# Optimization experiments

Measured on AMD Instinct MI355X. Metric: run time of the kernel, lower is better.

Reference implementation:

```python
import jax, jax.numpy as jnp
import numpy as np

B, SEQ, DIM = 4, 8192, 512
G = 32              # group_size: number of outer chunks (per source rearrange 'b (g n) d')
QK = 128            # query_key_dim
HD = QK // 4        # head_dim = 32 (used for softmax scale)
HEAD_D = 2 * HD     # per-head feature dim = 64 (h=2 heads over QK)
HID = DIM           # expansion_factor = 1.0
EPS = 1e-5


def _shift_seq(t):
    # F.pad(t, (0,0,1,-1)): prepend one zero row along axis=-2, drop last row
    pad = [(0, 0)] * (t.ndim - 2) + [(1, 0), (0, 0)]
    return jnp.pad(t, pad)[..., :-1, :]


def setup_inputs() -> dict:
    key = jax.random.key(0)
    ks = jax.random.split(key, 8)
    s = 0.02
    return {
        "x": jax.random.normal(ks[0], (B, SEQ, DIM), jnp.float32),
        "ln_g": jnp.ones((DIM,), jnp.float32),
        "ln_b": jnp.zeros((DIM,), jnp.float32),
        "w_qk": jax.random.normal(ks[1], (DIM, QK), jnp.float32) * s,
        "g4": jax.random.normal(ks[2], (4, QK), jnp.float32) * s,   # qk_offset_scale.gamma
        "b4": jnp.zeros((4, QK), jnp.float32),                       # qk_offset_scale.beta
        "g2": jax.random.normal(ks[3], (2, QK), jnp.float32) * s,   # shift_one_offset_scale.gamma
        "b2": jnp.zeros((2, QK), jnp.float32),
        "w_hidden": jax.random.normal(ks[4], (DIM, 2 * HID), jnp.float32) * s,
        "w_gate": jax.random.normal(ks[5], (DIM, HID), jnp.float32) * s,
        "w_out": jax.random.normal(ks[6], (5 * HID, DIM), jnp.float32) * s,
    }


def reference(x, ln_g, ln_b, w_qk, g4, b4, g2, b2, w_hidden, w_gate, w_out):
    b, seq, dim = x.shape
    n = seq // G  # tokens per chunk; seq chosen as multiple of G so padding = 0

    # LayerNorm
    mu = jnp.mean(x, axis=-1, keepdims=True)
    var = jnp.var(x, axis=-1, keepdims=True)
    xs = (x - mu) * jax.lax.rsqrt(var + EPS) * ln_g + ln_b

    # token shift of first half of channels (shift_tokens=True)
    half = dim // 2
    xs = jnp.concatenate([_shift_seq(xs[..., :half]), xs[..., half:]], axis=-1)

    qk = xs @ w_qk                                  # [b, seq, QK]
    qk_g = qk.reshape(b, G, n, QK)                  # 'b (g n) d -> b g n d', g outer
    qk_mean = qk_g.mean(axis=2)                     # [b, G, QK]

    # OffsetScale(heads=4) on per-chunk mean -> q_offset, k_offset, q_scale, k_scale
    offs = qk_mean[:, :, None, :] * g4 + b4         # [b, G, 4, QK]
    q_off, k_off, q_sc, k_sc = (offs[:, :, i, :] for i in range(4))

    q = qk_g * q_sc[:, :, None, :] + q_off[:, :, None, :]   # [b, G, n, QK]
    k = qk_g * k_sc[:, :, None, :] + k_off[:, :, None, :]

    # shift-by-one variants within each chunk, re-scaled + shift-one offsets
    q_s_off = qk_mean * g2[0] + b2[0]               # [b, G, QK]
    k_s_off = qk_mean * g2[1] + b2[1]
    qs = _shift_seq(q) * q_sc[:, :, None, :] + q_s_off[:, :, None, :]
    ks_ = _shift_seq(k) * k_sc[:, :, None, :] + k_s_off[:, :, None, :]

    def heads(t):  # [b,G,n,QK] -> [b,G,2,n,HEAD_D]
        return t.reshape(b, G, n, 2, HEAD_D).transpose(0, 1, 3, 2, 4)

    q_all = jnp.concatenate([heads(q), heads(qs)], axis=2)   # [b,G,4,n,64]
    k_all = jnp.concatenate([heads(k), heads(ks_)], axis=2)

    hg = xs @ w_hidden                              # [b, seq, 2*HID]
    hidden, gate = hg[..., :HID], hg[..., HID:]
    hidden_g = hidden.reshape(b, G, n, HID)

    sim = jnp.einsum('bghid,bghjd->bghij', q_all, k_all) * (HD ** -0.5)
    neg = -jnp.finfo(sim.dtype).max
    causal = jnp.triu(jnp.ones((n, n), dtype=bool), 1)  # applied unconditionally in source
    sim = jnp.where(causal, neg, sim)
    attn = jax.nn.softmax(sim, axis=-1)             # dropout=0 (eval)

    out = jnp.einsum('bghij,bgje->bghie', attn, hidden_g)   # [b,G,4,n,HID]
    gate_g = gate.reshape(b, G, n, HID)
    out = jax.nn.silu(out) * gate_g[:, :, None, :, :]
    out = out.transpose(0, 1, 3, 2, 4).reshape(b, seq, 4 * HID)  # 'b g h n e -> b (g n) (h e)'

    residual = jnp.concatenate([hidden, out], axis=-1)       # [b, seq, 5*HID]
    out = residual @ w_out                                   # [b, seq, dim]
    out = out * jax.nn.silu(xs @ w_gate)
    return out + xs
```

## Files before the change

kernel.cpp:

```cpp
#include <hip/hip_runtime.h>
#include <hip/hip_bf16.h>
#include <math.h>

#define BB 4
#define SEQ 8192
#define DIM 512
#define GG 32
#define NPG 256
#define QKD 128
#define HIDD 512

typedef unsigned short u16;
typedef unsigned int u32;

using s16x8 = __attribute__((ext_vector_type(8))) short;
using f32x4 = __attribute__((ext_vector_type(4))) float;

__device__ __forceinline__ float bf2f(u16 u) { return __uint_as_float(((u32)u) << 16); }
__device__ __forceinline__ u16 f2bf(float f) {
  u32 b = __float_as_uint(f);
  return (u16)((b + 0x7FFFu + ((b >> 16) & 1u)) >> 16);
}
__device__ __forceinline__ float silu_f(float x) { return x / (1.f + expf(-x)); }
__device__ __forceinline__ float silu_fast(float x) { return x / (1.f + __expf(-x)); }
__device__ __forceinline__ float4 fma4(float4 a, float4 b, float4 c) {
  return make_float4(a.x*b.x+c.x, a.y*b.y+c.y, a.z*b.z+c.z, a.w*b.w+c.w);
}
__device__ __forceinline__ float4 mul4(float4 a, float4 b) {
  return make_float4(a.x*b.x, a.y*b.y, a.z*b.z, a.w*b.w);
}
#define LD4(p, off) (*(const float4*)((p) + (off)))

__device__ __forceinline__ s16x8 aff8(s16x8 v, float4 s0, float4 s1, float4 o0, float4 o1) {
  union U { s16x8 x; u16 u[8]; };
  U in; in.x = v; U r;
  r.u[0] = f2bf(bf2f(in.u[0]) * s0.x + o0.x);
  r.u[1] = f2bf(bf2f(in.u[1]) * s0.y + o0.y);
  r.u[2] = f2bf(bf2f(in.u[2]) * s0.z + o0.z);
  r.u[3] = f2bf(bf2f(in.u[3]) * s0.w + o0.w);
  r.u[4] = f2bf(bf2f(in.u[4]) * s1.x + o1.x);
  r.u[5] = f2bf(bf2f(in.u[5]) * s1.y + o1.y);
  r.u[6] = f2bf(bf2f(in.u[6]) * s1.z + o1.z);
  r.u[7] = f2bf(bf2f(in.u[7]) * s1.w + o1.w);
  return r.x;
}
__device__ __forceinline__ s16x8 pack8(float4 a, float4 b) {
  union { s16x8 v; u16 u[8]; } z;
  z.u[0] = f2bf(a.x); z.u[1] = f2bf(a.y); z.u[2] = f2bf(a.z); z.u[3] = f2bf(a.w);
  z.u[4] = f2bf(b.x); z.u[5] = f2bf(b.y); z.u[6] = f2bf(b.z); z.u[7] = f2bf(b.w);
  return z.v;
}

__global__ __launch_bounds__(256) void k_ln(const float* __restrict__ x,
    const float* __restrict__ lg, const float* __restrict__ lb, float* __restrict__ xs) {
  const int row = blockIdx.x;
  const int s = row & (SEQ - 1);
  const int t = threadIdx.x;
  const float* xr = x + (size_t)row * DIM;
  float v0 = xr[t], v1 = xr[t + 256];
  float sum = v0 + v1, sq = v0 * v0 + v1 * v1;
  #pragma unroll
  for (int o = 32; o; o >>= 1) { sum += __shfl_down(sum, o); sq += __shfl_down(sq, o); }
  __shared__ float sm[8];
  const int w = t >> 6;
  if ((t & 63) == 0) { sm[w] = sum; sm[4 + w] = sq; }
  __syncthreads();
  if (t == 0) {
    float S = sm[0] + sm[1] + sm[2] + sm[3];
    float Q = sm[4] + sm[5] + sm[6] + sm[7];
    float mu = S * (1.f / DIM);
    float var = Q * (1.f / DIM) - mu * mu;
    sm[0] = mu; sm[4] = rsqrtf(var + 1e-5f);
  }
  __syncthreads();
  const float mu = sm[0], rs = sm[4];
  float y0 = (v0 - mu) * rs * lg[t] + lb[t];
  float y1 = (v1 - mu) * rs * lg[t + 256] + lb[t + 256];
  xs[(size_t)row * DIM + t + 256] = y1;
  if (s + 1 < SEQ) xs[(size_t)(row + 1) * DIM + t] = y0;
  if (s == 0) xs[(size_t)row * DIM + t] = 0.f;
}

__global__ __launch_bounds__(256) void k_trw(const float* __restrict__ src, u16* __restrict__ dst,
    int N, int dstLD, int rowOff) {
  __shared__ u16 T[64][66];
  const int t = threadIdx.x;
  const int k0 = blockIdx.x * 64, n0 = blockIdx.y * 64;
  #pragma unroll
  for (int i = 0; i < 16; ++i) {
    int idx = t + 256 * i;
    int r = idx >> 6, c = idx & 63;
    T[c][r] = f2bf(src[(size_t)(k0 + r) * N + n0 + c]);
  }
  __syncthreads();
  #pragma unroll
  for (int i = 0; i < 16; ++i) {
    int idx = t + 256 * i;
    int r = idx >> 6, c = idx & 63;
    dst[(size_t)(rowOff + n0 + r) * dstLD + k0 + c] = T[r][c];
  }
}

__global__ __launch_bounds__(256) void k_trh(const u16* __restrict__ hidt, u16* __restrict__ hidr) {
  __shared__ u16 T[64][66];
  const int t = threadIdx.x;
  const int j0 = blockIdx.x * 64;
  const int e0 = blockIdx.y * 64;
  const int bg = blockIdx.z;
  #pragma unroll
  for (int i = 0; i < 16; ++i) {
    int idx = t + 256 * i; int r = idx >> 6, c = idx & 63;
    T[c][r] = hidt[((size_t)bg * 512 + e0 + r) * 256 + j0 + c];
  }
  __syncthreads();
  #pragma unroll
  for (int i = 0; i < 16; ++i) {
    int idx = t + 256 * i; int r = idx >> 6, c = idx & 63;
    hidr[((size_t)bg * 256 + j0 + r) * 512 + e0 + c] = T[r][c];
  }
}

__global__ __launch_bounds__(256, 2) void k_gemm1m(const float* __restrict__ xs,
    const u16* __restrict__ w1t, u16* __restrict__ qk, u16* __restrict__ hidt,
    u16* __restrict__ gate, u16* __restrict__ xg) {
  __shared__ u16 As[128][72];
  __shared__ u16 Bs[128][72];
  const int t = threadIdx.x;
  const int m0 = blockIdx.x * 128, n0 = blockIdx.y * 128;
  const int w = t >> 6, l = t & 63, lr = l & 15, lq = l >> 4;
  const int wr = (w >> 1) * 64, wc = (w & 1) * 64;
  const int sr = t >> 3;
  const int sk = (t & 7) * 8;
  f32x4 acc[4][4];
  #pragma unroll
  for (int i = 0; i < 4; ++i)
    #pragma unroll
    for (int j = 0; j < 4; ++j) acc[i][j] = (f32x4){0.f, 0.f, 0.f, 0.f};
  for (int k0 = 0; k0 < 512; k0 += 64) {
    s16x8 aS[4], bS[4];
    #pragma unroll
    for (int it = 0; it < 4; ++it) {
      const float* ap = xs + (size_t)(m0 + sr + it * 32) * 512 + k0 + sk;
      float4 f0 = *(const float4*)ap;
      float4 f1 = *(const float4*)(ap + 4);
      s16x8 v;
      v[0] = (short)f2bf(f0.x); v[1] = (short)f2bf(f0.y); v[2] = (short)f2bf(f0.z); v[3] = (short)f2bf(f0.w);
      v[4] = (short)f2bf(f1.x); v[5] = (short)f2bf(f1.y); v[6] = (short)f2bf(f1.z); v[7] = (short)f2bf(f1.w);
      aS[it] = v;
      bS[it] = *(const s16x8*)(w1t + (size_t)(n0 + sr + it * 32) * 512 + k0 + sk);
    }
    __syncthreads();
    #pragma unroll
    for (int it = 0; it < 4; ++it) {
      *(s16x8*)&As[sr + it * 32][sk] = aS[it];
      *(s16x8*)&Bs[sr + it * 32][sk] = bS[it];
    }
    __syncthreads();
    #pragma unroll
    for (int kk = 0; kk < 64; kk += 32) {
      s16x8 af[4], bf[4];
      #pragma unroll
      for (int fi = 0; fi < 4; ++fi) af[fi] = *(const s16x8*)&As[wr + fi * 16 + lr][kk + 8 * lq];
      #pragma unroll
      for (int fj = 0; fj < 4; ++fj) bf[fj] = *(const s16x8*)&Bs[wc + fj * 16 + lr][kk + 8 * lq];
      #pragma unroll
      for (int fi = 0; fi < 4; ++fi)
        #pragma unroll
        for (int fj = 0; fj < 4; ++fj)
          acc[fi][fj] = __builtin_amdgcn_mfma_f32_16x16x32_bf16(af[fi], bf[fj], acc[fi][fj], 0, 0, 0);
    }
  }
  if (n0 == 0) {
    #pragma unroll
    for (int fi = 0; fi < 4; ++fi)
      #pragma unroll
      for (int fj = 0; fj < 4; ++fj) {
        const int n = wc + fj * 16 + lr;
        const int mb = m0 + wr + fi * 16 + lq * 4;
        #pragma unroll
        for (int r = 0; r < 4; ++r)
          qk[(size_t)(mb + r) * QKD + n] = f2bf(acc[fi][fj][r]);
      }
  } else if (n0 < 640) {
    const int bg = m0 >> 8;
    #pragma unroll
    for (int fi = 0; fi < 4; ++fi)
      #pragma unroll
      for (int fj = 0; fj < 4; ++fj) {
        const int e = n0 - 128 + wc + fj * 16 + lr;
        const int j0 = (m0 & 255) + wr + fi * 16 + lq * 4;
        ushort4 pk;
        pk.x = f2bf(acc[fi][fj][0]); pk.y = f2bf(acc[fi][fj][1]);
        pk.z = f2bf(acc[fi][fj][2]); pk.w = f2bf(acc[fi][fj][3]);
        *(ushort4*)(hidt + ((size_t)bg * 512 + e) * 256 + j0) = pk;
      }
  } else if (n0 < 1152) {
    #pragma unroll
    for (int fi = 0; fi < 4; ++fi)
      #pragma unroll
      for (int fj = 0; fj < 4; ++fj) {
        const int n = n0 - 640 + wc + fj * 16 + lr;
        const int mb = m0 + wr + fi * 16 + lq * 4;
        #pragma unroll
        for (int r = 0; r < 4; ++r)
          gate[(size_t)(mb + r) * HIDD + n] = f2bf(acc[fi][fj][r]);
      }
  } else {
    #pragma unroll
    for (int fi = 0; fi < 4; ++fi)
      #pragma unroll
      for (int fj = 0; fj < 4; ++fj) {
        const int n = n0 - 1152 + wc + fj * 16 + lr;
        const int mb = m0 + wr + fi * 16 + lq * 4;
        #pragma unroll
        for (int r = 0; r < 4; ++r)
          xg[(size_t)(mb + r) * HIDD + n] = f2bf(silu_f(acc[fi][fj][r]));
      }
  }
}

__global__ __launch_bounds__(128) void k_qkmean(const u16* __restrict__ qk, float* __restrict__ qm) {
  const int bg = blockIdx.x;
  const int c = threadIdx.x;
  const u16* p = qk + (size_t)bg * NPG * QKD + c;
  float s = 0.f;
  for (int i = 0; i < NPG; ++i) s += bf2f(p[(size_t)i * QKD]);
  qm[(size_t)bg * QKD + c] = s * (1.f / NPG);
}

__global__ __launch_bounds__(256, 4) void k_attn(const u16* __restrict__ qk,
    const float* __restrict__ qm, const float* __restrict__ g4, const float* __restrict__ b4,
    const float* __restrict__ g2, const float* __restrict__ b2,
    const u16* __restrict__ hidt, const u16* __restrict__ gate, u16* __restrict__ out4) {
  __shared__ u16 Vs[64][264];
  const int t = threadIdx.x;
  const int l = t & 63;
  const int h = t >> 6;
  const bool sh = (h >= 2);
  const int blk = blockIdx.x;
  const int xcd = blk & 7;
  const int bb = blk >> 3;
  const int bg = xcd * 16 + (bb >> 4);
  const int iw = 15 - (bb & 15);
  const size_t grpRow = (size_t)bg * NPG;
  const int cbase = (h & 1) << 6;
  const int lr = l & 15, lq = l >> 4;
  const int cA = cbase + 8 * lq;
  const int ntmax = iw, jtmax = iw >> 1;
  const int irow = iw * 16 + lr;
  const float* qmp = qm + bg * QKD;
  float4 qmA = LD4(qmp, cA),      qmB = LD4(qmp, cA + 4);
  float4 qmC = LD4(qmp, cA + 32), qmD = LD4(qmp, cA + 36);
  float4 qscA = fma4(qmA, LD4(g4, 2*QKD+cA),    LD4(b4, 2*QKD+cA));
  float4 qscB = fma4(qmB, LD4(g4, 2*QKD+cA+4),  LD4(b4, 2*QKD+cA+4));
  float4 qscC = fma4(qmC, LD4(g4, 2*QKD+cA+32), LD4(b4, 2*QKD+cA+32));
  float4 qscD = fma4(qmD, LD4(g4, 2*QKD+cA+36), LD4(b4, 2*QKD+cA+36));
  float4 qofA = fma4(qmA, LD4(g4, cA),      LD4(b4, cA));
  float4 qofB = fma4(qmB, LD4(g4, cA+4),    LD4(b4, cA+4));
  float4 qofC = fma4(qmC, LD4(g4, cA+32),   LD4(b4, cA+32));
  float4 qofD = fma4(qmD, LD4(g4, cA+36),   LD4(b4, cA+36));
  float4 kscA = fma4(qmA, LD4(g4, 3*QKD+cA),    LD4(b4, 3*QKD+cA));
  float4 kscB = fma4(qmB, LD4(g4, 3*QKD+cA+4),  LD4(b4, 3*QKD+cA+4));
  float4 kscC = fma4(qmC, LD4(g4, 3*QKD+cA+32), LD4(b4, 3*QKD+cA+32));
  float4 kscD = fma4(qmD, LD4(g4, 3*QKD+cA+36), LD4(b4, 3*QKD+cA+36));
  float4 kofA = fma4(qmA, LD4(g4, QKD+cA),      LD4(b4, QKD+cA));
  float4 kofB = fma4(qmB, LD4(g4, QKD+cA+4),    LD4(b4, QKD+cA+4));
  float4 kofC = fma4(qmC, LD4(g4, QKD+cA+32),   LD4(b4, QKD+cA+32));
  float4 kofD = fma4(qmD, LD4(g4, QKD+cA+36),   LD4(b4, QKD+cA+36));
  s16x8 qz0 = {0,0,0,0,0,0,0,0}, qz1 = qz0, kz0 = qz0, kz1 = qz0;
  if (sh) {
    float4 qsoA = fma4(qmA, LD4(g2, cA),    LD4(b2, cA));
    float4 qsoB = fma4(qmB, LD4(g2, cA+4),  LD4(b2, cA+4));
    float4 qsoC = fma4(qmC, LD4(g2, cA+32), LD4(b2, cA+32));
    float4 qsoD = fma4(qmD, LD4(g2, cA+36), LD4(b2, cA+36));
    float4 ksoA = fma4(qmA, LD4(g2, QKD+cA),    LD4(b2, QKD+cA));
    float4 ksoB = fma4(qmB, LD4(g2, QKD+cA+4),  LD4(b2, QKD+cA+4));
    float4 ksoC = fma4(qmC, LD4(g2, QKD+cA+32), LD4(b2, QKD+cA+32));
    float4 ksoD = fma4(qmD, LD4(g2, QKD+cA+36), LD4(b2, QKD+cA+36));
    qofA = fma4(qofA, qscA, qsoA); qofB = fma4(qofB, qscB, qsoB);
    qofC = fma4(qofC, qscC, qsoC); qofD = fma4(qofD, qscD, qsoD);
    qscA = mul4(qscA, qscA); qscB = mul4(qscB, qscB);
    qscC = mul4(qscC, qscC); qscD = mul4(qscD, qscD);
    kofA = fma4(kofA, kscA, ksoA); kofB = fma4(kofB, kscB, ksoB);
    kofC = fma4(kofC, kscC, ksoC); kofD = fma4(kofD, kscD, ksoD);
    kscA = mul4(kscA, kscA); kscB = mul4(kscB, kscB);
    kscC = mul4(kscC, kscC); kscD = mul4(kscD, kscD);
    qz0 = pack8(qsoA, qsoB); qz1 = pack8(qsoC, qsoD);
    kz0 = pack8(ksoA, ksoB); kz1 = pack8(ksoC, ksoD);
  }
  const float scl = 0.17677669529663687f;
  const int qsrc = sh ? (irow ? irow - 1 : 0) : irow;
  const u16* qrow = qk + (grpRow + qsrc) * QKD + cA;
  s16x8 qb0 = aff8(*(const s16x8*)qrow,        qscA, qscB, qofA, qofB);
  s16x8 qb1 = aff8(*(const s16x8*)(qrow + 32), qscC, qscD, qofC, qofD);
  if (sh && irow == 0) { qb0 = qz0; qb1 = qz1; }
  f32x4 sfr[16];
  #pragma unroll
  for (int nt = 0; nt < 16; ++nt) if (nt <= ntmax) {
    const int jr = nt * 16 + lr;
    const int ksrc = sh ? (jr ? jr - 1 : 0) : jr;
    const u16* kr = qk + (grpRow + ksrc) * QKD + cA;
    s16x8 ka0 = aff8(*(const s16x8*)kr,        kscA, kscB, kofA, kofB);
    s16x8 ka1 = aff8(*(const s16x8*)(kr + 32), kscC, kscD, kofC, kofD);
    if (sh && jr == 0) { ka0 = kz0; ka1 = kz1; }
    f32x4 c = {0.f, 0.f, 0.f, 0.f};
    c = __builtin_amdgcn_mfma_f32_16x16x32_bf16(ka0, qb0, c, 0, 0, 0);
    c = __builtin_amdgcn_mfma_f32_16x16x32_bf16(ka1, qb1, c, 0, 0, 0);
    sfr[nt] = c;
  }
  float mx = -3.4e38f;
  #pragma unroll
  for (int nt = 0; nt < 16; ++nt) if (nt <= ntmax) {
    #pragma unroll
    for (int r = 0; r < 4; ++r) {
      int j = nt * 16 + lq * 4 + r;
      if (j <= irow) mx = fmaxf(mx, sfr[nt][r] * scl);
    }
  }
  mx = fmaxf(mx, __shfl_xor(mx, 16));
  mx = fmaxf(mx, __shfl_xor(mx, 32));
  float sum = 0.f;
  u32 p01[16], p23[16];
  #pragma unroll
  for (int nt = 0; nt < 16; ++nt) { p01[nt] = 0u; p23[nt] = 0u; }
  #pragma unroll
  for (int nt = 0; nt < 16; ++nt) if (nt <= ntmax) {
    int j = nt * 16 + lq * 4;
    float e0 = (j + 0 <= irow) ? __expf(sfr[nt][0] * scl - mx) : 0.f;
    float e1 = (j + 1 <= irow) ? __expf(sfr[nt][1] * scl - mx) : 0.f;
    float e2 = (j + 2 <= irow) ? __expf(sfr[nt][2] * scl - mx) : 0.f;
    float e3 = (j + 3 <= irow) ? __expf(sfr[nt][3] * scl - mx) : 0.f;
    sum += (e0 + e1) + (e2 + e3);
    p01[nt] = (u32)f2bf(e0) | ((u32)f2bf(e1) << 16);
    p23[nt] = (u32)f2bf(e2) | ((u32)f2bf(e3) << 16);
  }
  sum += __shfl_xor(sum, 16);
  sum += __shfl_xor(sum, 32);
  const float inv = 1.f / sum;
  const int srcA = (l & 15) | ((l & 16) << 1);
  const int srcB = srcA + 16;
  const bool hi = (l >= 32);
  s16x8 bfr[8];
  #pragma unroll
  for (int jt = 0; jt < 8; ++jt) if (jt <= jtmax) {
    u32 a0 = __shfl((int)p01[2 * jt], srcA), a1 = __shfl((int)p23[2 * jt], srcA);
    u32 a2 = __shfl((int)p01[2 * jt], srcB), a3 = __shfl((int)p23[2 * jt], srcB);
    u32 b0 = __shfl((int)p01[2 * jt + 1], srcA), b1 = __shfl((int)p23[2 * jt + 1], srcA);
    u32 b2 = __shfl((int)p01[2 * jt + 1], srcB), b3 = __shfl((int)p23[2 * jt + 1], srcB);
    union { u32 u[4]; s16x8 v; } bb2;
    bb2.u[0] = hi ? b0 : a0; bb2.u[1] = hi ? b1 : a1;
    bb2.u[2] = hi ? b2 : a2; bb2.u[3] = hi ? b3 : a3;
    bfr[jt] = bb2.v;
  }
  const u16* vtb = hidt + (size_t)bg * (512 * 256);
  const size_t srow = grpRow + irow;
  const u16* gp = gate + srow * HIDD;
  u16* op = out4 + srow * 2048 + ((size_t)h << 9);
  for (int oct = 0; oct < 8; ++oct) {
    __syncthreads();
    const u16* src = vtb + (size_t)oct * 64 * 256;
    #pragma unroll
    for (int it = 0; it < 8; ++it) {
      int flat = it * 256 + t;
      int row = flat >> 5, col8 = (flat & 31) * 8;
      *(uint4*)&Vs[row][col8] = *(const uint4*)(src + (size_t)row * 256 + col8);
    }
    __syncthreads();
    f32x4 acc[4];
    #pragma unroll
    for (int ef = 0; ef < 4; ++ef) acc[ef] = (f32x4){0.f, 0.f, 0.f, 0.f};
    #pragma unroll
    for (int jt = 0; jt < 8; ++jt) if (jt <= jtmax) {
      __builtin_amdgcn_s_setprio(1);
      #pragma unroll
      for (int ef = 0; ef < 4; ++ef) {
        s16x8 va = *(const s16x8*)&Vs[ef * 16 + lr][jt * 32 + 8 * lq];
        acc[ef] = __builtin_amdgcn_mfma_f32_16x16x32_bf16(va, bfr[jt], acc[ef], 0, 0, 0);
      }
      __builtin_amdgcn_s_setprio(0);
    }
    #pragma unroll
    for (int ef = 0; ef < 4; ++ef) {
      const int e = oct * 64 + ef * 16 + lq * 4;
      ushort4 gu = *(const ushort4*)(gp + e);
      ushort4 ov;
      ov.x = f2bf(silu_fast(acc[ef][0] * inv) * bf2f(gu.x));
      ov.y = f2bf(silu_fast(acc[ef][1] * inv) * bf2f(gu.y));
      ov.z = f2bf(silu_fast(acc[ef][2] * inv) * bf2f(gu.z));
      ov.w = f2bf(silu_fast(acc[ef][3] * inv) * bf2f(gu.w));
      *(ushort4*)(op + e) = ov;
    }
  }
}

__global__ __launch_bounds__(256, 2) void k_gemm2m(const u16* __restrict__ hidr,
    const u16* __restrict__ out4, const u16* __restrict__ wt,
    const u16* __restrict__ xg, float* __restrict__ out) {
  __shared__ u16 As[128][72];
  __shared__ u16 Bs[128][72];
  const int t = threadIdx.x;
  const int m0 = blockIdx.x * 128, n0 = blockIdx.y * 128;
  const int w = t >> 6, l = t & 63, lr = l & 15, lq = l >> 4;
  const int wr = (w >> 1) * 64, wc = (w & 1) * 64;
  const int sr = t >> 3;
  const int sk = (t & 7) * 8;
  f32x4 acc[4][4];
  #pragma unroll
  for (int i = 0; i < 4; ++i)
    #pragma unroll
    for (int j = 0; j < 4; ++j) acc[i][j] = (f32x4){0.f, 0.f, 0.f, 0.f};
  for (int k0 = 0; k0 < 2560; k0 += 64) {
    const u16* abase; size_t ald; int koff;
    if (k0 < 512) { abase = hidr; ald = 512; koff = k0; }
    else          { abase = out4; ald = 2048; koff = k0 - 512; }
    s16x8 aS[4], bS[4];
    #pragma unroll
    for (int it = 0; it < 4; ++it) {
      aS[it] = *(const s16x8*)(abase + (size_t)(m0 + sr + it * 32) * ald + koff + sk);
      bS[it] = *(const s16x8*)(wt + (size_t)(n0 + sr + it * 32) * 2560 + k0 + sk);
    }
    __syncthreads();
    #pragma unroll
    for (int it = 0; it < 4; ++it) {
      *(s16x8*)&As[sr + it * 32][sk] = aS[it];
      *(s16x8*)&Bs[sr + it * 32][sk] = bS[it];
    }
    __syncthreads();
    #pragma unroll
    for (int kk = 0; kk < 64; kk += 32) {
      s16x8 af[4], bf[4];
      #pragma unroll
      for (int fi = 0; fi < 4; ++fi) af[fi] = *(const s16x8*)&As[wr + fi * 16 + lr][kk + 8 * lq];
      #pragma unroll
      for (int fj = 0; fj < 4; ++fj) bf[fj] = *(const s16x8*)&Bs[wc + fj * 16 + lr][kk + 8 * lq];
      #pragma unroll
      for (int fi = 0; fi < 4; ++fi)
        #pragma unroll
        for (int fj = 0; fj < 4; ++fj)
          acc[fi][fj] = __builtin_amdgcn_mfma_f32_16x16x32_bf16(af[fi], bf[fj], acc[fi][fj], 0, 0, 0);
    }
  }
  #pragma unroll
  for (int fi = 0; fi < 4; ++fi)
    #pragma unroll
    for (int fj = 0; fj < 4; ++fj) {
      const int n = n0 + wc + fj * 16 + lr;
      const int mb = m0 + wr + fi * 16 + lq * 4;
      #pragma unroll
      for (int r = 0; r < 4; ++r) {
        const size_t idx = (size_t)(mb + r) * DIM + n;
        out[idx] = acc[fi][fj][r] * bf2f(xg[idx]) + out[idx];
      }
    }
}

extern "C" void kernel_launch(void* const* d_in, const int* in_sizes, int n_in,
                              void* d_out, int out_size, void* d_ws, size_t ws_size,
                              hipStream_t stream) {
  const float* x        = (const float*)d_in[0];
  const float* lg       = (const float*)d_in[1];
  const float* lb       = (const float*)d_in[2];
  const float* w_qk     = (const float*)d_in[3];
  const float* g4       = (const float*)d_in[4];
  const float* b4       = (const float*)d_in[5];
  const float* g2       = (const float*)d_in[6];
  const float* b2       = (const float*)d_in[7];
  const float* w_hidden = (const float*)d_in[8];
  const float* w_gate   = (const float*)d_in[9];
  const float* w_out    = (const float*)d_in[10];
  if (ws_size < 247660544ull) return;
  char* ws = (char*)d_ws;
  float* QM   = (float*)(ws + 0);
  u16*   HIDT = (u16*)  (ws + 65536);
  u16*   GATE = (u16*)  (ws + 33619968);
  u16*   XG   = (u16*)  (ws + 67174400);
  u16*   QKb  = (u16*)  (ws + 100728832);
  u16*   W1T  = (u16*)  (ws + 109117440);
  u16*   WT   = (u16*)  (ws + 110821376);
  u16*   OUT4 = (u16*)  (ws + 113442816);
  u16*   HIDR = (u16*)  (ws + 33619968);
  float* XS   = (float*)d_out;
  float* OUT  = (float*)d_out;

  k_ln<<<BB * SEQ, 256, 0, stream>>>(x, lg, lb, XS);
  k_trw<<<dim3(8, 2),  256, 0, stream>>>(w_qk,     W1T, 128,  512,  0);
  k_trw<<<dim3(8, 16), 256, 0, stream>>>(w_hidden, W1T, 1024, 512,  128);
  k_trw<<<dim3(8, 8),  256, 0, stream>>>(w_gate,   W1T, 512,  512,  1152);
  k_trw<<<dim3(40, 8), 256, 0, stream>>>(w_out,    WT,  512,  2560, 0);
  k_gemm1m<<<dim3(256, 13), 256, 0, stream>>>(XS, W1T, QKb, HIDT, GATE, XG);
  k_qkmean<<<BB * GG, 128, 0, stream>>>(QKb, QM);
  k_attn<<<BB * GG * 16, 256, 0, stream>>>(QKb, QM, g4, b4, g2, b2, HIDT, GATE, OUT4);
  k_trh<<<dim3(4, 8, 128), 256, 0, stream>>>(HIDT, HIDR);
  k_gemm2m<<<dim3(256, 4), 256, 0, stream>>>(HIDR, OUT4, WT, XG, OUT);
}
```

Before: 457.1 us.

## Double-buffer GEMM LDS tiles, swizzle blocks per XCD, emit bf16 LN output

Both GEMM kernels now use two LDS buffers, so the global loads for tile k+2 and the LDS stores for tile k+1 overlap with the MFMA work on tile k, leaving one barrier per iteration. Block indices are remapped so each XCD gets a contiguous range of M rows, which is meant to improve L2 reuse. LayerNorm also writes a bf16 copy of xs, so GEMM1 reads half the bytes and skips per-tile conversion. This doubles LDS use, which may limit occupancy, and the XSB buffer aliases OUT4, relying on k_attn writing OUT4 only after GEMM1 has consumed XSB.

```diff
diff --git a/kernel.cpp b/kernel.cpp
--- a/kernel.cpp
+++ b/kernel.cpp
@@ -52,7 +52,8 @@
 }
 
 __global__ __launch_bounds__(256) void k_ln(const float* __restrict__ x,
-    const float* __restrict__ lg, const float* __restrict__ lb, float* __restrict__ xs) {
+    const float* __restrict__ lg, const float* __restrict__ lb,
+    float* __restrict__ xs, u16* __restrict__ xsb) {
   const int row = blockIdx.x;
   const int s = row & (SEQ - 1);
   const int t = threadIdx.x;
@@ -77,8 +78,12 @@
   float y0 = (v0 - mu) * rs * lg[t] + lb[t];
   float y1 = (v1 - mu) * rs * lg[t + 256] + lb[t + 256];
   xs[(size_t)row * DIM + t + 256] = y1;
-  if (s + 1 < SEQ) xs[(size_t)(row + 1) * DIM + t] = y0;
-  if (s == 0) xs[(size_t)row * DIM + t] = 0.f;
+  xsb[(size_t)row * DIM + t + 256] = f2bf(y1);
+  if (s + 1 < SEQ) {
+    xs[(size_t)(row + 1) * DIM + t] = y0;
+    xsb[(size_t)(row + 1) * DIM + t] = f2bf(y0);
+  }
+  if (s == 0) { xs[(size_t)row * DIM + t] = 0.f; xsb[(size_t)row * DIM + t] = 0; }
 }
 
 __global__ __launch_bounds__(256) void k_trw(const float* __restrict__ src, u16* __restrict__ dst,
@@ -120,13 +125,17 @@
   }
 }
 
-__global__ __launch_bounds__(256, 2) void k_gemm1m(const float* __restrict__ xs,
+__global__ __launch_bounds__(256, 2) void k_gemm1m(const u16* __restrict__ xsb,
     const u16* __restrict__ w1t, u16* __restrict__ qk, u16* __restrict__ hidt,
     u16* __restrict__ gate, u16* __restrict__ xg) {
-  __shared__ u16 As[128][72];
-  __shared__ u16 Bs[128][72];
+  __shared__ u16 As[2][128][72];
+  __shared__ u16 Bs[2][128][72];
   const int t = threadIdx.x;
-  const int m0 = blockIdx.x * 128, n0 = blockIdx.y * 128;
+  const int blk = blockIdx.x;
+  const int xcd = blk & 7;
+  const int loc = blk >> 3;
+  const int m0 = (xcd * 32 + loc / 13) * 128;
+  const int n0 = (loc % 13) * 128;
   const int w = t >> 6, l = t & 63, lr = l & 15, lq = l >> 4;
   const int wr = (w >> 1) * 64, wc = (w & 1) * 64;
   const int sr = t >> 3;
@@ -136,40 +145,47 @@
   for (int i = 0; i < 4; ++i)
     #pragma unroll
     for (int j = 0; j < 4; ++j) acc[i][j] = (f32x4){0.f, 0.f, 0.f, 0.f};
-  for (int k0 = 0; k0 < 512; k0 += 64) {
-    s16x8 aS[4], bS[4];
-    #pragma unroll
-    for (int it = 0; it < 4; ++it) {
-      const float* ap = xs + (size_t)(m0 + sr + it * 32) * 512 + k0 + sk;
-      float4 f0 = *(const float4*)ap;
-      float4 f1 = *(const float4*)(ap + 4);
-      s16x8 v;
-      v[0] = (short)f2bf(f0.x); v[1] = (short)f2bf(f0.y); v[2] = (short)f2bf(f0.z); v[3] = (short)f2bf(f0.w);
-      v[4] = (short)f2bf(f1.x); v[5] = (short)f2bf(f1.y); v[6] = (short)f2bf(f1.z); v[7] = (short)f2bf(f1.w);
-      aS[it] = v;
-      bS[it] = *(const s16x8*)(w1t + (size_t)(n0 + sr + it * 32) * 512 + k0 + sk);
-    }
-    __syncthreads();
-    #pragma unroll
-    for (int it = 0; it < 4; ++it) {
-      *(s16x8*)&As[sr + it * 32][sk] = aS[it];
-      *(s16x8*)&Bs[sr + it * 32][sk] = bS[it];
-    }
-    __syncthreads();
+  s16x8 rA[4], rB[4];
+#define G1LOAD(T) { const int k0_ = (T) * 64;                                        \
+    _Pragma("unroll")                                                                \
+    for (int it = 0; it < 4; ++it) {                                                 \
+      rA[it] = *(const s16x8*)(xsb + (size_t)(m0 + sr + it * 32) * 512 + k0_ + sk);  \
+      rB[it] = *(const s16x8*)(w1t + (size_t)(n0 + sr + it * 32) * 512 + k0_ + sk);  \
+    } }
+  G1LOAD(0);
+  #pragma unroll
+  for (int it = 0; it < 4; ++it) {
+    *(s16x8*)&As[0][sr + it * 32][sk] = rA[it];
+    *(s16x8*)&Bs[0][sr + it * 32][sk] = rB[it];
+  }
+  G1LOAD(1);
+  __syncthreads();
+  for (int tt = 0; tt < 8; ++tt) {
+    const int cur = tt & 1;
+    if (tt + 1 < 8) {
+      #pragma unroll
+      for (int it = 0; it < 4; ++it) {
+        *(s16x8*)&As[cur ^ 1][sr + it * 32][sk] = rA[it];
+        *(s16x8*)&Bs[cur ^ 1][sr + it * 32][sk] = rB[it];
+      }
+      if (tt + 2 < 8) G1LOAD(tt + 2);
+    }
     #pragma unroll
     for (int kk = 0; kk < 64; kk += 32) {
       s16x8 af[4], bf[4];
       #pragma unroll
-      for (int fi = 0; fi < 4; ++fi) af[fi] = *(const s16x8*)&As[wr + fi * 16 + lr][kk + 8 * lq];
-      #pragma unroll
-      for (int fj = 0; fj < 4; ++fj) bf[fj] = *(const s16x8*)&Bs[wc + fj * 16 + lr][kk + 8 * lq];
+      for (int fi = 0; fi < 4; ++fi) af[fi] = *(const s16x8*)&As[cur][wr + fi * 16 + lr][kk + 8 * lq];
+      #pragma unroll
+      for (int fj = 0; fj < 4; ++fj) bf[fj] = *(const s16x8*)&Bs[cur][wc + fj * 16 + lr][kk + 8 * lq];
       #pragma unroll
       for (int fi = 0; fi < 4; ++fi)
         #pragma unroll
         for (int fj = 0; fj < 4; ++fj)
           acc[fi][fj] = __builtin_amdgcn_mfma_f32_16x16x32_bf16(af[fi], bf[fj], acc[fi][fj], 0, 0, 0);
     }
-  }
+    __syncthreads();
+  }
+#undef G1LOAD
   if (n0 == 0) {
     #pragma unroll
     for (int fi = 0; fi < 4; ++fi)
@@ -396,10 +412,14 @@
 __global__ __launch_bounds__(256, 2) void k_gemm2m(const u16* __restrict__ hidr,
     const u16* __restrict__ out4, const u16* __restrict__ wt,
     const u16* __restrict__ xg, float* __restrict__ out) {
-  __shared__ u16 As[128][72];
-  __shared__ u16 Bs[128][72];
+  __shared__ u16 As[2][128][72];
+  __shared__ u16 Bs[2][128][72];
   const int t = threadIdx.x;
-  const int m0 = blockIdx.x * 128, n0 = blockIdx.y * 128;
+  const int blk = blockIdx.x;
+  const int xcd = blk & 7;
+  const int loc = blk >> 3;
+  const int m0 = (xcd * 32 + (loc >> 2)) * 128;
+  const int n0 = (loc & 3) * 128;
   const int w = t >> 6, l = t & 63, lr = l & 15, lq = l >> 4;
   const int wr = (w >> 1) * 64, wc = (w & 1) * 64;
   const int sr = t >> 3;
@@ -409,37 +429,50 @@
   for (int i = 0; i < 4; ++i)
     #pragma unroll
     for (int j = 0; j < 4; ++j) acc[i][j] = (f32x4){0.f, 0.f, 0.f, 0.f};
-  for (int k0 = 0; k0 < 2560; k0 += 64) {
-    const u16* abase; size_t ald; int koff;
-    if (k0 < 512) { abase = hidr; ald = 512; koff = k0; }
-    else          { abase = out4; ald = 2048; koff = k0 - 512; }
-    s16x8 aS[4], bS[4];
-    #pragma unroll
-    for (int it = 0; it < 4; ++it) {
-      aS[it] = *(const s16x8*)(abase + (size_t)(m0 + sr + it * 32) * ald + koff + sk);
-      bS[it] = *(const s16x8*)(wt + (size_t)(n0 + sr + it * 32) * 2560 + k0 + sk);
-    }
-    __syncthreads();
-    #pragma unroll
-    for (int it = 0; it < 4; ++it) {
-      *(s16x8*)&As[sr + it * 32][sk] = aS[it];
-      *(s16x8*)&Bs[sr + it * 32][sk] = bS[it];
-    }
-    __syncthreads();
+  s16x8 rA[4], rB[4];
+#define G2LOAD(T) { const int k0_ = (T) * 64;                                        \
+    const u16* ab_; size_t ald_; int ko_;                                            \
+    if (k0_ < 512) { ab_ = hidr; ald_ = 512; ko_ = k0_; }                            \
+    else           { ab_ = out4; ald_ = 2048; ko_ = k0_ - 512; }                     \
+    _Pragma("unroll")                                                                \
+    for (int it = 0; it < 4; ++it) {                                                 \
+      rA[it] = *(const s16x8*)(ab_ + (size_t)(m0 + sr + it * 32) * ald_ + ko_ + sk); \
+      rB[it] = *(const s16x8*)(wt + (size_t)(n0 + sr + it * 32) * 2560 + k0_ + sk);  \
+    } }
+  G2LOAD(0);
+  #pragma unroll
+  for (int it = 0; it < 4; ++it) {
+    *(s16x8*)&As[0][sr + it * 32][sk] = rA[it];
+    *(s16x8*)&Bs[0][sr + it * 32][sk] = rB[it];
+  }
+  G2LOAD(1);
+  __syncthreads();
+  for (int tt = 0; tt < 40; ++tt) {
+    const int cur = tt & 1;
+    if (tt + 1 < 40) {
+      #pragma unroll
+      for (int it = 0; it < 4; ++it) {
+        *(s16x8*)&As[cur ^ 1][sr + it * 32][sk] = rA[it];
+        *(s16x8*)&Bs[cur ^ 1][sr + it * 32][sk] = rB[it];
+      }
+      if (tt + 2 < 40) G2LOAD(tt + 2);
+    }
     #pragma unroll
     for (int kk = 0; kk < 64; kk += 32) {
       s16x8 af[4], bf[4];
       #pragma unroll
-      for (int fi = 0; fi < 4; ++fi) af[fi] = *(const s16x8*)&As[wr + fi * 16 + lr][kk + 8 * lq];
-      #pragma unroll
-      for (int fj = 0; fj < 4; ++fj) bf[fj] = *(const s16x8*)&Bs[wc + fj * 16 + lr][kk + 8 * lq];
+      for (int fi = 0; fi < 4; ++fi) af[fi] = *(const s16x8*)&As[cur][wr + fi * 16 + lr][kk + 8 * lq];
+      #pragma unroll
+      for (int fj = 0; fj < 4; ++fj) bf[fj] = *(const s16x8*)&Bs[cur][wc + fj * 16 + lr][kk + 8 * lq];
       #pragma unroll
       for (int fi = 0; fi < 4; ++fi)
         #pragma unroll
         for (int fj = 0; fj < 4; ++fj)
           acc[fi][fj] = __builtin_amdgcn_mfma_f32_16x16x32_bf16(af[fi], bf[fj], acc[fi][fj], 0, 0, 0);
     }
-  }
+    __syncthreads();
+  }
+#undef G2LOAD
   #pragma unroll
   for (int fi = 0; fi < 4; ++fi)
     #pragma unroll
@@ -478,18 +511,19 @@
   u16*   W1T  = (u16*)  (ws + 109117440);
   u16*   WT   = (u16*)  (ws + 110821376);
   u16*   OUT4 = (u16*)  (ws + 113442816);
+  u16*   XSB  = (u16*)  (ws + 113442816);
   u16*   HIDR = (u16*)  (ws + 33619968);
   float* XS   = (float*)d_out;
   float* OUT  = (float*)d_out;
 
-  k_ln<<<BB * SEQ, 256, 0, stream>>>(x, lg, lb, XS);
+  k_ln<<<BB * SEQ, 256, 0, stream>>>(x, lg, lb, XS, XSB);
   k_trw<<<dim3(8, 2),  256, 0, stream>>>(w_qk,     W1T, 128,  512,  0);
   k_trw<<<dim3(8, 16), 256, 0, stream>>>(w_hidden, W1T, 1024, 512,  128);
   k_trw<<<dim3(8, 8),  256, 0, stream>>>(w_gate,   W1T, 512,  512,  1152);
   k_trw<<<dim3(40, 8), 256, 0, stream>>>(w_out,    WT,  512,  2560, 0);
-  k_gemm1m<<<dim3(256, 13), 256, 0, stream>>>(XS, W1T, QKb, HIDT, GATE, XG);
+  k_gemm1m<<<3328, 256, 0, stream>>>(XSB, W1T, QKb, HIDT, GATE, XG);
   k_qkmean<<<BB * GG, 128, 0, stream>>>(QKb, QM);
   k_attn<<<BB * GG * 16, 256, 0, stream>>>(QKb, QM, g4, b4, g2, b2, HIDT, GATE, OUT4);
   k_trh<<<dim3(4, 8, 128), 256, 0, stream>>>(HIDT, HIDR);
-  k_gemm2m<<<dim3(256, 4), 256, 0, stream>>>(HIDR, OUT4, WT, XG, OUT);
-}
+  k_gemm2m<<<1024, 256, 0, stream>>>(HIDR, OUT4, WT, XG, OUT);
+}
```

Result: faster. 436.6 us (-4.5%).
